# Optimization experiments

Measured on AMD Instinct MI355X. Metric: run time of the kernel, lower is better.

## Reference

```python
import jax, jax.numpy as jnp
import numpy as np

# ---- model hyperparameters (match init_kwargs) ----
N_ATOMS = 16000
N_EDGES = 256000
F = 128          # n_atom_basis
NF = 32          # n_filters
L = 3            # n_interactions
N_RBF = 20
CUTOFF = 5.0
MAX_Z = 100
INV_SQRT_F = np.float32(1.0 / np.sqrt(F))
INV_SQRT_2NF = np.float32(1.0 / np.sqrt(2 * NF))
SQ2 = np.float32(np.sqrt(2.0)); SQ3 = np.float32(np.sqrt(3.0)); SQ6 = np.float32(np.sqrt(6.0))
LOG2 = np.float32(np.log(2.0))


def ssp(x):
    # shifted softplus: softplus(x) - log(2)
    return jax.nn.softplus(x) - LOG2


def setup_inputs() -> dict:
    key = jax.random.key(0)
    k = jax.random.split(key, 16)
    Z = jax.random.randint(k[0], (N_ATOMS,), 0, MAX_Z)
    r_ij = jax.random.normal(k[1], (N_EDGES, 3), dtype=jnp.float32) * 2.0
    idx_i = jnp.sort(jax.random.randint(k[2], (N_EDGES,), 0, N_ATOMS))
    idx_j = jax.random.randint(k[3], (N_EDGES,), 0, N_ATOMS)
    # parameters (e3nn Linear: N(0,1) weights with explicit 1/sqrt(fan_in) in the math;
    # filter-network Dense: fan-in scaled weights, zero bias; padding_idx=0 -> zero row)
    emb = jax.random.normal(k[4], (MAX_Z, F), dtype=jnp.float32).at[0].set(0.0)
    W_pe = jax.random.normal(k[5], (F, F), dtype=jnp.float32)
    W0s = jax.random.normal(k[6], (L, F, NF), dtype=jnp.float32)   # in2f, 0e path
    W0v = jax.random.normal(k[7], (L, F, NF), dtype=jnp.float32)   # in2f, 1o path
    Wf1 = jax.random.normal(k[8], (L, N_RBF, NF), dtype=jnp.float32) / np.sqrt(N_RBF)
    bf1 = jnp.zeros((L, NF), jnp.float32)
    Wf2 = jax.random.normal(k[9], (L, NF, 6 * NF), dtype=jnp.float32) / np.sqrt(NF)
    bf2 = jnp.zeros((L, 6 * NF), jnp.float32)
    As = jax.random.normal(k[10], (L, 2 * NF, F), dtype=jnp.float32)  # f2out_1 0e
    Av = jax.random.normal(k[11], (L, 2 * NF, F), dtype=jnp.float32)  # f2out_1 1o
    Bs = jax.random.normal(k[12], (L, F, F), dtype=jnp.float32)       # f2out_2 0e
    Bv = jax.random.normal(k[13], (L, F, F), dtype=jnp.float32)       # f2out_2 1o
    return dict(Z=Z, r_ij=r_ij, idx_i=idx_i, idx_j=idx_j, emb=emb, W_pe=W_pe,
                W0s=W0s, W0v=W0v, Wf1=Wf1, bf1=bf1, Wf2=Wf2, bf2=bf2,
                As=As, Av=Av, Bs=Bs, Bv=Bv)


def _interaction(xs, xv, idx_i, idx_j, f_ij, rcut, Yv,
                 W0s, W0v, Wf1, bf1, Wf2, bf2, As, Av, Bs, Bv):
    n_atoms = xs.shape[0]
    # in2f: e3nn o3.Linear (per-l channel mixing, fan-in normalized)
    hs = (xs @ W0s) * INV_SQRT_F                        # [N, NF]  (0e)
    hv = jnp.einsum('nfc,fg->ngc', xv, W0v) * INV_SQRT_F  # [N, NF, 3] (1o)
    sj = hs[idx_j]                                      # gather neighbors [E, NF]
    vj = hv[idx_j]                                      # [E, NF, 3]
    # FullTensorProduct (0e+1o) x Y(0e+1o); Y0 = 1, Y1 = sqrt(3)*r_hat (component norm)
    Yb = Yv[:, None, :]                                 # [E, 1, 3]
    t0a = sj                                            # 0e x 0e -> 0e
    t0b = jnp.einsum('efc,ec->ef', vj, Yv) / SQ3        # 1o x 1o -> 0e
    t1a = sj[:, :, None] * Yb                           # 0e x 1o -> 1o
    t1b = vj                                            # 1o x 0e -> 1o
    t1e = jnp.cross(vj, Yb) / SQ2                       # 1o x 1o -> 1e
    ux, uy, uz = vj[..., 0], vj[..., 1], vj[..., 2]
    wx, wy, wz = Yv[:, None, 0], Yv[:, None, 1], Yv[:, None, 2]
    t2e = jnp.stack([(ux * wy + uy * wx) / SQ2,         # 1o x 1o -> 2e (sym traceless)
                     (uy * wz + uz * wy) / SQ2,
                     (2 * uz * wz - ux * wx - uy * wy) / SQ6,
                     (ux * wz + uz * wx) / SQ2,
                     (ux * wx - uy * wy) / SQ2], axis=-1)  # [E, NF, 5]
    # filter network + cutoff envelope: W_ij [E, 6*NF] (one scalar per irrep)
    W = (ssp(f_ij @ Wf1 + bf1) @ Wf2 + bf2) * rcut[:, None]
    w0a, w0b, w1a, w1b, w1e, w2e = jnp.split(W, 6, axis=1)
    E = sj.shape[0]
    # elementwise tensor product (scale each irrep by its scalar), then scatter-add
    y_all = jnp.concatenate([
        t0a * w0a, t0b * w0b,
        (t1a * w1a[..., None]).reshape(E, -1),
        (t1b * w1b[..., None]).reshape(E, -1),
        (t1e * w1e[..., None]).reshape(E, -1),
        (t2e * w2e[..., None]).reshape(E, -1)], axis=1)   # [E, 16*NF]
    agg = jax.ops.segment_sum(y_all, idx_i, num_segments=n_atoms)  # [N, 16*NF]
    s_in = agg[:, :2 * NF]
    v_in = agg[:, 2 * NF:8 * NF].reshape(n_atoms, 2 * NF, 3)
    # f2out_1: output irreps are F x (0e+1o) -> 1e and 2e channels have no path (dropped)
    os = ssp((s_in @ As) * INV_SQRT_2NF)                # f2out_1 + scalar activation
    ov = jnp.einsum('nfc,fg->ngc', v_in, Av) * INV_SQRT_2NF
    os = (os @ Bs) * INV_SQRT_F                         # f2out_2
    ov = jnp.einsum('nfc,fg->ngc', ov, Bv) * INV_SQRT_F
    return os, ov


def _forward(Z, r_ij, idx_i, idx_j, emb, W_pe, W0s, W0v, Wf1, bf1, Wf2, bf2, As, Av, Bs, Bv):
    xs = (emb[Z] @ W_pe) * INV_SQRT_F                   # embedding + post_embedding (0e)
    xv = jnp.zeros((xs.shape[0], F, 3), xs.dtype)       # 1o part starts at zero (no 0e->1o path)
    d = jnp.linalg.norm(r_ij, axis=1)
    offsets = jnp.linspace(0.0, CUTOFF, N_RBF).astype(jnp.float32)
    coeff = -0.5 / (offsets[1] - offsets[0]) ** 2
    f_ij = jnp.exp(coeff * (d[:, None] - offsets) ** 2)  # Gaussian RBF [E, N_RBF]
    rcut = 0.5 * (jnp.cos(np.float32(np.pi) * d / CUTOFF) + 1.0) * (d < CUTOFF)
    # spherical harmonics, normalize=True + component normalization (Y0=1, Y1=sqrt(3)*rhat);
    # the r_ij*rcut prescaling in the original doesn't change the direction, and edges with
    # rcut=0 contribute nothing since W_ij carries the rcut factor.
    Yv = SQ3 * r_ij / jnp.maximum(d, 1e-9)[:, None]
    for l in range(L):
        vs, vv = _interaction(xs, xv, idx_i, idx_j, f_ij, rcut, Yv,
                              W0s[l], W0v[l], Wf1[l], bf1[l], Wf2[l], bf2[l],
                              As[l], Av[l], Bs[l], Bv[l])
        xs = xs + vs
        xv = xv + vv
    return xs  # scalar_representation [N, F]


def reference(Z, r_ij, idx_i, idx_j, emb, W_pe, W0s, W0v, Wf1, bf1, Wf2, bf2, As, Av, Bs, Bv):
    return _forward(Z, r_ij, idx_i, idx_j, emb, W_pe, W0s, W0v, Wf1, bf1, Wf2, bf2, As, Av, Bs, Bv)
```

## Files before the change

### kernel.cpp

```cpp
#include <hip/hip_runtime.h>
#include <math.h>

constexpr int NA   = 16000;
constexpr int NE   = 256000;
constexpr int F    = 128;
constexpr int NF   = 32;
constexpr int NRBF = 20;
constexpr float CUTOFF       = 5.0f;
constexpr float INV_SQRT_F   = 0.0883883476483184f;
constexpr float INV_SQRT_2NF = 0.125f;
constexpr float INV_SQ3      = 0.5773502691896258f;
constexpr float SQ3          = 1.7320508075688772f;
constexpr float LOG2_        = 0.6931471805599453f;
constexpr float PI_          = 3.14159265358979323f;

typedef _Float16 h2 __attribute__((ext_vector_type(2)));

__device__ __forceinline__ float ssp(float x) {
    return fmaxf(x, 0.0f) + __logf(1.0f + __expf(-fabsf(x))) - LOG2_;
}
__device__ __forceinline__ float fdot2(h2 a, h2 b, float c) {
#if __has_builtin(__builtin_amdgcn_fdot2)
    return __builtin_amdgcn_fdot2(a, b, c, false);
#else
    return c + (float)a[0]*(float)b[0] + (float)a[1]*(float)b[1];
#endif
}

__global__ void geom_kernel(const float* __restrict__ r_ij,
                            float* __restrict__ fijT,
                            float* __restrict__ yvrT) {
    int e = blockIdx.x * blockDim.x + threadIdx.x;
    if (e >= NE) return;
    float x = r_ij[3*e+0], y = r_ij[3*e+1], z = r_ij[3*e+2];
    float d = sqrtf(x*x + y*y + z*z);
    const float delta = CUTOFF / (NRBF - 1);
    const float coeff = -0.5f / (delta * delta);
    #pragma unroll
    for (int k = 0; k < NRBF; k++) {
        float t = d - delta * (float)k;
        fijT[(size_t)k*NE + e] = __expf(coeff * t * t);
    }
    float rc = 0.5f * (__cosf(PI_ * d / CUTOFF) + 1.0f);
    rc = (d < CUTOFF) ? rc : 0.0f;
    float inv = SQ3 / fmaxf(d, 1e-9f);
    yvrT[0*(size_t)NE + e] = x * inv;
    yvrT[1*(size_t)NE + e] = y * inv;
    yvrT[2*(size_t)NE + e] = z * inv;
    yvrT[3*(size_t)NE + e] = rc;
}

__global__ void preph_kernel(const float* __restrict__ Wf2, const float* __restrict__ Wf1,
                             h2* __restrict__ Wf2H, h2* __restrict__ Wf1H) {
    int u = blockIdx.x * 256 + threadIdx.x;
    if (u < 3*128*16) {
        int l = u / (128*16), rem = u % (128*16), c = rem >> 4, k2 = rem & 15;
        const float* W = Wf2 + (size_t)l*NF*192;
        Wf2H[u] = h2{(_Float16)W[(2*k2)*192 + c], (_Float16)W[(2*k2+1)*192 + c]};
    }
    if (u < 3*320) {
        int l = u / 320, rem = u % 320, k2 = rem >> 5, g = rem & 31;
        const float* W = Wf1 + (size_t)l*NRBF*NF;
        Wf1H[u] = h2{(_Float16)W[(2*k2)*32 + g], (_Float16)W[(2*k2+1)*32 + g]};
    }
}

__global__ void prep2_kernel(const float* __restrict__ Av, const float* __restrict__ Bv,
                             float* __restrict__ AvBv) {
    int u = blockIdx.x * 256 + threadIdx.x;
    if (u >= 3*64*128) return;
    int l = u >> 13, rem = u & 8191, f = rem >> 7, c = rem & 127;
    const float* av = Av + (size_t)l*64*128 + f*128;
    const float* bv = Bv + (size_t)l*128*128 + c;
    float acc = 0.f;
    #pragma unroll 8
    for (int g = 0; g < 128; g++) acc += av[g] * bv[(size_t)g*128];
    AvBv[u] = acc * (INV_SQRT_2NF * INV_SQRT_F);
}

__global__ __launch_bounds__(256, 4)
void embed_kernel(const int* __restrict__ Z,
                  const float* __restrict__ emb,
                  const float* __restrict__ Wpe,
                  float* __restrict__ xs) {
    __shared__ float ER[32][128];
    __shared__ int   Zs[32];
    int t = threadIdx.x;
    int a0 = blockIdx.x * 32;
    if (t < 32) Zs[t] = Z[a0 + t];
    __syncthreads();
    {
        const float4* emb4 = (const float4*)emb;
        float4* ER4 = (float4*)&ER[0][0];
        #pragma unroll
        for (int it = 0; it < 4; it++) {
            int u4 = it*256 + t;
            int a = u4 >> 5, k4 = u4 & 31;
            ER4[u4] = emb4[(size_t)Zs[a]*32 + k4];
        }
    }
    __syncthreads();
    int c = t & 127, half = t >> 7;
    float acc[16];
    #pragma unroll
    for (int a = 0; a < 16; a++) acc[a] = 0.f;
    for (int k = 0; k < 128; k++) {
        float w = Wpe[k*128 + c];
        #pragma unroll
        for (int a = 0; a < 16; a++) acc[a] += ER[half*16 + a][k] * w;
    }
    #pragma unroll
    for (int a = 0; a < 16; a++)
        xs[(size_t)(a0 + half*16 + a)*128 + c] = acc[a] * INV_SQRT_F;
}

template <bool XV_ZERO>
__global__ __launch_bounds__(256, 4)
void h_kernel(const float* __restrict__ xs,
              const float* __restrict__ xv,
              const float* __restrict__ W0s,
              const float* __restrict__ W0v,
              float* __restrict__ hsv) {
    __shared__ float X[16][512];
    int t = threadIdx.x;
    int a0 = blockIdx.x * 16;
    {
        float* Xf = &X[0][0];
        const float4* xs4 = (const float4*)xs;
        #pragma unroll
        for (int it = 0; it < 2; it++) {
            int u4 = it*256 + t;
            int a = u4 >> 5, k4 = u4 & 31;
            *(float4*)&Xf[a*512 + k4*4] = xs4[(size_t)a0*32 + u4];
        }
        if (!XV_ZERO) {
            const float4* xv4 = (const float4*)xv;
            #pragma unroll
            for (int it = 0; it < 6; it++) {
                int u4 = it*256 + t;
                int a = u4 / 96, rem = u4 - a*96;
                *(float4*)&Xf[a*512 + 128 + rem*4] = xv4[(size_t)a0*96 + u4];
            }
        }
    }
    __syncthreads();
    int g = t & 31, r = t >> 5;
    int sel = r & 3, half = r >> 2;
    if (XV_ZERO && sel != 0) {
        #pragma unroll
        for (int a = 0; a < 8; a++) {
            int n = a0 + half*8 + a;
            hsv[(size_t)n*128 + 32 + g*3 + (sel-1)] = 0.f;
        }
        return;
    }
    const float* W = (sel == 0) ? W0s : W0v;
    int xoff = (sel == 0) ? 0 : (128 + (sel-1)*128);
    float acc[8];
    #pragma unroll
    for (int a = 0; a < 8; a++) acc[a] = 0.f;
    for (int k = 0; k < 128; k++) {
        float w = W[k*32 + g];
        #pragma unroll
        for (int a = 0; a < 8; a++) acc[a] += X[half*8 + a][xoff + k] * w;
    }
    #pragma unroll
    for (int a = 0; a < 8; a++) {
        int n = a0 + half*8 + a;
        if (sel == 0) hsv[(size_t)n*128 + g] = acc[a] * INV_SQRT_F;
        else          hsv[(size_t)n*128 + 32 + g*3 + (sel-1)] = acc[a] * INV_SQRT_F;
    }
}

template <bool DO_V>
__global__ __launch_bounds__(256, 6)
void agg_kernel(const int* __restrict__ idx_i,
                const int* __restrict__ idx_j,
                const float* __restrict__ fijT,
                const float* __restrict__ yvrT,
                const float* __restrict__ hsv,
                const h2* __restrict__ Wf1H,
                const float* __restrict__ bf1,
                const h2* __restrict__ Wf2H,
                const float* __restrict__ bf2,
                float* __restrict__ aggG) {
    __shared__ h2 LW1[320];
    __shared__ h2 HB[4][64][18];
    int t = threadIdx.x;
    for (int u = t; u < 320; u += 256) LW1[u] = Wf1H[u];
    __syncthreads();

    int wid = t >> 6, lane = t & 63;
    int base = (blockIdx.x*4 + wid) * 64;

    int   il = idx_i[base + lane];
    int   jl = idx_j[base + lane];
    float y0l = yvrT[0*(size_t)NE + base + lane];
    float y1l = yvrT[1*(size_t)NE + base + lane];
    float y2l = yvrT[2*(size_t)NE + base + lane];
    float y3l = yvrT[3*(size_t)NE + base + lane];

    int ilp = __shfl_up(il, 1);
    unsigned long long bmask = __ballot(lane > 0 && il != ilp);

    h2 fp[10];
    #pragma unroll
    for (int k2 = 0; k2 < 10; k2++) {
        float fa = fijT[(size_t)(2*k2)*NE + base + lane];
        float fb = fijT[(size_t)(2*k2+1)*NE + base + lane];
        fp[k2] = h2{(_Float16)fa, (_Float16)fb};
    }
    float h[32];
    #pragma unroll
    for (int g = 0; g < 32; g++) h[g] = bf1[g];
    #pragma unroll
    for (int k2 = 0; k2 < 10; k2++) {
        #pragma unroll
        for (int g = 0; g < 32; g++)
            h[g] = fdot2(fp[k2], LW1[k2*32 + g], h[g]);
    }
    #pragma unroll
    for (int g = 0; g < 32; g++) h[g] = ssp(h[g]);
    #pragma unroll
    for (int i = 0; i < 16; i++)
        HB[wid][lane][i] = h2{(_Float16)h[2*i], (_Float16)h[2*i+1]};

    h2 w2a[16], w2b[16];
    #pragma unroll
    for (int k2 = 0; k2 < 16; k2++) w2a[k2] = Wf2H[lane*16 + k2];
    if (DO_V) {
        #pragma unroll
        for (int k2 = 0; k2 < 16; k2++) w2b[k2] = Wf2H[(64+lane)*16 + k2];
    }
    float bf2a = bf2[lane];
    float bf2b = DO_V ? bf2[64 + lane] : 0.f;

    int idxQ = 32 + 3*(lane - 32);

    float a0 = 0.f, a1 = 0.f, a2 = 0.f, a3 = 0.f;
    int prev = __builtin_amdgcn_readlane(il, 0);

    for (int ii = 0; ii < 64; ++ii) {
        if ((bmask >> ii) & 1ull) {
            unsafeAtomicAdd(&aggG[(size_t)prev*256 + lane], a0);
            a0 = 0.f;
            if (DO_V) {
                unsafeAtomicAdd(&aggG[(size_t)prev*256 + 64 + lane],  a1);
                unsafeAtomicAdd(&aggG[(size_t)prev*256 + 128 + lane], a2);
                unsafeAtomicAdd(&aggG[(size_t)prev*256 + 192 + lane], a3);
                a1 = a2 = a3 = 0.f;
            }
            prev = __builtin_amdgcn_readlane(il, ii);
        }
        int j = __builtin_amdgcn_readlane(jl, ii);
        const float* row = hsv + (size_t)j*128;
        float q0, q1, q2;
        if (lane < 32) {
            q0 = row[lane]; q1 = q0; q2 = q0;
        } else {
            const float* p = row + idxQ;
            q0 = p[0]; q1 = p[1]; q2 = p[2];
        }
        float s0 = bf2a, s1 = bf2b;
        const h2* hrow = &HB[wid][ii][0];
        #pragma unroll
        for (int k2 = 0; k2 < 16; k2++) {
            h2 hq = hrow[k2];
            s0 = fdot2(hq, w2a[k2], s0);
            if (DO_V) s1 = fdot2(hq, w2b[k2], s1);
        }
        float y3s = __int_as_float(__builtin_amdgcn_readlane(__float_as_int(y3l), ii));
        float y0s = __int_as_float(__builtin_amdgcn_readlane(__float_as_int(y0l), ii));
        float y1s = __int_as_float(__builtin_amdgcn_readlane(__float_as_int(y1l), ii));
        float y2s = __int_as_float(__builtin_amdgcn_readlane(__float_as_int(y2l), ii));
        float w0 = s0 * y3s;
        float dot = (q0*y0s + q1*y1s + q2*y2s) * INV_SQ3;
        float v0 = (lane < 32) ? q0 : dot;
        a0 += v0 * w0;
        if (DO_V) {
            float w1 = s1 * y3s;
            float m1 = (lane < 32) ? y0s : 1.0f;
            float m2 = (lane < 32) ? y1s : 1.0f;
            float m3 = (lane < 32) ? y2s : 1.0f;
            a1 += q0 * m1 * w1;
            a2 += q1 * m2 * w1;
            a3 += q2 * m3 * w1;
        }
    }
    unsafeAtomicAdd(&aggG[(size_t)prev*256 + lane], a0);
    if (DO_V) {
        unsafeAtomicAdd(&aggG[(size_t)prev*256 + 64 + lane],  a1);
        unsafeAtomicAdd(&aggG[(size_t)prev*256 + 128 + lane], a2);
        unsafeAtomicAdd(&aggG[(size_t)prev*256 + 192 + lane], a3);
    }
}

template <bool DO_V, bool XV_WRITE>
__global__ __launch_bounds__(256, 4)
void mlp_kernel(const float* __restrict__ aggG,
                const float* __restrict__ As,
                const float* __restrict__ Bs,
                const float* __restrict__ AvBv,
                float* __restrict__ xs,
                float* __restrict__ xv) {
    constexpr int AC = DO_V ? 256 : 64;
    __shared__ float aggL[16][AC];
    __shared__ float outL[16][128];
    int t = threadIdx.x;
    int a0 = blockIdx.x * 16;
    {
        const float4* g4 = (const float4*)(aggG + (size_t)a0*256);
        if (DO_V) {
            float4* l4 = (float4*)&aggL[0][0];
            #pragma unroll
            for (int it = 0; it < 4; it++) l4[it*256 + t] = g4[it*256 + t];
        } else {
            int row = t >> 4, c4 = t & 15;
            *(float4*)&aggL[row][c4*4] = g4[row*64 + c4];
        }
    }
    __syncthreads();

    int q  = t & 31;
    int rp = t >> 5;
    const float4* As4 = (const float4*)As;
    const float4* Bs4 = (const float4*)Bs;

    {
        float ox0=0,oy0=0,oz0=0,ow0=0, ox1=0,oy1=0,oz1=0,ow1=0;
        const float4* x0p = (const float4*)&aggL[rp][0];
        const float4* x1p = (const float4*)&aggL[rp+8][0];
        #pragma unroll 4
        for (int kq = 0; kq < 16; kq++) {
            float4 x0 = x0p[kq], x1 = x1p[kq];
            float4 wa = As4[(4*kq+0)*32 + q];
            float4 wb = As4[(4*kq+1)*32 + q];
            float4 wc = As4[(4*kq+2)*32 + q];
            float4 wd = As4[(4*kq+3)*32 + q];
            ox0 += x0.x*wa.x + x0.y*wb.x + x0.z*wc.x + x0.w*wd.x;
            oy0 += x0.x*wa.y + x0.y*wb.y + x0.z*wc.y + x0.w*wd.y;
            oz0 += x0.x*wa.z + x0.y*wb.z + x0.z*wc.z + x0.w*wd.z;
            ow0 += x0.x*wa.w + x0.y*wb.w + x0.z*wc.w + x0.w*wd.w;
            ox1 += x1.x*wa.x + x1.y*wb.x + x1.z*wc.x + x1.w*wd.x;
            oy1 += x1.x*wa.y + x1.y*wb.y + x1.z*wc.y + x1.w*wd.y;
            oz1 += x1.x*wa.z + x1.y*wb.z + x1.z*wc.z + x1.w*wd.z;
            ow1 += x1.x*wa.w + x1.y*wb.w + x1.z*wc.w + x1.w*wd.w;
        }
        float4 r0 = { ssp(ox0*INV_SQRT_2NF), ssp(oy0*INV_SQRT_2NF), ssp(oz0*INV_SQRT_2NF), ssp(ow0*INV_SQRT_2NF) };
        float4 r1 = { ssp(ox1*INV_SQRT_2NF), ssp(oy1*INV_SQRT_2NF), ssp(oz1*INV_SQRT_2NF), ssp(ow1*INV_SQRT_2NF) };
        *(float4*)&outL[rp][4*q]   = r0;
        *(float4*)&outL[rp+8][4*q] = r1;
    }
    if (DO_V) {
        const float4* AB4 = (const float4*)AvBv;
        int ra[6], rc[6];
        #pragma unroll
        for (int i = 0; i < 6; i++) {
            int rv = rp + 8*i;
            ra[i] = rv/3; rc[i] = rv - 3*(rv/3);
        }
        float o[6][4];
        #pragma unroll
        for (int i = 0; i < 6; i++) { o[i][0]=0; o[i][1]=0; o[i][2]=0; o[i][3]=0; }
        const float4* vp[6];
        #pragma unroll
        for (int i = 0; i < 6; i++)
            vp[i] = (const float4*)&aggL[ra[i]][64 + rc[i]*64];
        #pragma unroll 2
        for (int kq = 0; kq < 16; kq++) {
            float4 wa = AB4[(4*kq+0)*32 + q];
            float4 wb = AB4[(4*kq+1)*32 + q];
            float4 wc = AB4[(4*kq+2)*32 + q];
            float4 wd = AB4[(4*kq+3)*32 + q];
            #pragma unroll
            for (int i = 0; i < 6; i++) {
                float4 x = vp[i][kq];
                o[i][0] += x.x*wa.x + x.y*wb.x + x.z*wc.x + x.w*wd.x;
                o[i][1] += x.x*wa.y + x.y*wb.y + x.z*wc.y + x.w*wd.y;
                o[i][2] += x.x*wa.z + x.y*wb.z + x.z*wc.z + x.w*wd.z;
                o[i][3] += x.x*wa.w + x.y*wb.w + x.z*wc.w + x.w*wd.w;
            }
        }
        #pragma unroll
        for (int i = 0; i < 6; i++) {
            float4* p = (float4*)&xv[(size_t)(a0+ra[i])*384 + rc[i]*128 + 4*q];
            if (XV_WRITE) {
                float4 c = { o[i][0], o[i][1], o[i][2], o[i][3] };
                *p = c;
            } else {
                float4 c = *p;
                c.x += o[i][0]; c.y += o[i][1]; c.z += o[i][2]; c.w += o[i][3];
                *p = c;
            }
        }
    }
    __syncthreads();
    {
        float ox0=0,oy0=0,oz0=0,ow0=0, ox1=0,oy1=0,oz1=0,ow1=0;
        const float4* x0p = (const float4*)&outL[rp][0];
        const float4* x1p = (const float4*)&outL[rp+8][0];
        #pragma unroll 4
        for (int kq = 0; kq < 32; kq++) {
            float4 x0 = x0p[kq], x1 = x1p[kq];
            float4 wa = Bs4[(4*kq+0)*32 + q];
            float4 wb = Bs4[(4*kq+1)*32 + q];
            float4 wc = Bs4[(4*kq+2)*32 + q];
            float4 wd = Bs4[(4*kq+3)*32 + q];
            ox0 += x0.x*wa.x + x0.y*wb.x + x0.z*wc.x + x0.w*wd.x;
            oy0 += x0.x*wa.y + x0.y*wb.y + x0.z*wc.y + x0.w*wd.y;
            oz0 += x0.x*wa.z + x0.y*wb.z + x0.z*wc.z + x0.w*wd.z;
            ow0 += x0.x*wa.w + x0.y*wb.w + x0.z*wc.w + x0.w*wd.w;
            ox1 += x1.x*wa.x + x1.y*wb.x + x1.z*wc.x + x1.w*wd.x;
            oy1 += x1.x*wa.y + x1.y*wb.y + x1.z*wc.y + x1.w*wd.y;
            oz1 += x1.x*wa.z + x1.y*wb.z + x1.z*wc.z + x1.w*wd.z;
            ow1 += x1.x*wa.w + x1.y*wb.w + x1.z*wc.w + x1.w*wd.w;
        }
        float4* p0 = (float4*)&xs[(size_t)(a0+rp)*128 + 4*q];
        float4* p1 = (float4*)&xs[(size_t)(a0+rp+8)*128 + 4*q];
        float4 c0 = *p0, c1 = *p1;
        c0.x += ox0*INV_SQRT_F; c0.y += oy0*INV_SQRT_F; c0.z += oz0*INV_SQRT_F; c0.w += ow0*INV_SQRT_F;
        c1.x += ox1*INV_SQRT_F; c1.y += oy1*INV_SQRT_F; c1.z += oz1*INV_SQRT_F; c1.w += ow1*INV_SQRT_F;
        *p0 = c0; *p1 = c1;
    }
}

extern "C" void kernel_launch(void* const* d_in, const int* in_sizes, int n_in,
                              void* d_out, int out_size, void* d_ws, size_t ws_size,
                              hipStream_t stream) {
    (void)in_sizes; (void)n_in; (void)out_size; (void)ws_size;
    const int*   Z     = (const int*)  d_in[0];
    const float* r_ij  = (const float*)d_in[1];
    const int*   idx_i = (const int*)  d_in[2];
    const int*   idx_j = (const int*)  d_in[3];
    const float* emb   = (const float*)d_in[4];
    const float* Wpe   = (const float*)d_in[5];
    const float* W0s   = (const float*)d_in[6];
    const float* W0v   = (const float*)d_in[7];
    const float* Wf1   = (const float*)d_in[8];
    const float* bf1   = (const float*)d_in[9];
    const float* Wf2   = (const float*)d_in[10];
    const float* bf2   = (const float*)d_in[11];
    const float* As    = (const float*)d_in[12];
    const float* Av    = (const float*)d_in[13];
    const float* Bs    = (const float*)d_in[14];
    const float* Bv    = (const float*)d_in[15];

    float* xs = (float*)d_out;
    float* ws = (float*)d_ws;
    float* fijT = ws;
    float* yvrT = fijT + (size_t)NE*NRBF;
    float* xv   = yvrT + (size_t)NE*4;
    float* hsv  = xv   + (size_t)NA*F*3;
    float* aggG = hsv  + (size_t)NA*F;
    float* AvBv = aggG + (size_t)NA*256;
    h2*    Wf2H = (h2*)(AvBv + (size_t)3*64*128);
    h2*    Wf1H = Wf2H + (size_t)3*128*16;

    geom_kernel<<<(NE+255)/256, 256, 0, stream>>>(r_ij, fijT, yvrT);
    preph_kernel<<<24, 256, 0, stream>>>(Wf2, Wf1, Wf2H, Wf1H);
    prep2_kernel<<<(3*64*128+255)/256, 256, 0, stream>>>(Av, Bv, AvBv);
    embed_kernel<<<NA/32, 256, 0, stream>>>(Z, emb, Wpe, xs);

    for (int l = 0; l < 3; l++) {
        if (l == 0)
            h_kernel<true><<<NA/16, 256, 0, stream>>>(xs, xv,
                W0s + (size_t)l*F*NF, W0v + (size_t)l*F*NF, hsv);
        else
            h_kernel<false><<<NA/16, 256, 0, stream>>>(xs, xv,
                W0s + (size_t)l*F*NF, W0v + (size_t)l*F*NF, hsv);

        hipMemsetAsync(aggG, 0, (size_t)NA*256*sizeof(float), stream);

        if (l < 2)
            agg_kernel<true><<<NE/256, 256, 0, stream>>>(idx_i, idx_j, fijT, yvrT, hsv,
                Wf1H + (size_t)l*320, bf1 + (size_t)l*NF,
                Wf2H + (size_t)l*128*16, bf2 + (size_t)l*6*NF, aggG);
        else
            agg_kernel<false><<<NE/256, 256, 0, stream>>>(idx_i, idx_j, fijT, yvrT, hsv,
                Wf1H + (size_t)l*320, bf1 + (size_t)l*NF,
                Wf2H + (size_t)l*128*16, bf2 + (size_t)l*6*NF, aggG);

        if (l == 0)
            mlp_kernel<true, true><<<NA/16, 256, 0, stream>>>(aggG,
                As + (size_t)l*2*NF*F, Bs + (size_t)l*F*F, AvBv + (size_t)l*64*128, xs, xv);
        else if (l == 1)
            mlp_kernel<true, false><<<NA/16, 256, 0, stream>>>(aggG,
                As + (size_t)l*2*NF*F, Bs + (size_t)l*F*F, AvBv + (size_t)l*64*128, xs, xv);
        else
            mlp_kernel<false, false><<<NA/16, 256, 0, stream>>>(aggG,
                As + (size_t)l*2*NF*F, Bs + (size_t)l*F*F, AvBv + (size_t)l*64*128, xs, xv);
    }
}
```

Before: 400.0 us.

## Fuse next-layer filter projection into embed and MLP kernels, vectorize agg row loads

Removes the separate h_kernel by computing the in2f projection (hsv) at the tail of embed_kernel for layer 0 and at the tail of mlp_kernel for later layers, reusing the freshly updated xs/xv rows already held in shared memory. This avoids re-reading xs and xv from global memory and saves three kernel launches. The agg kernel's per-edge filter hidden rows are also stored and read as 16-byte vectors. Launch bounds are relaxed (agg to 4 and mlp to 3 waves per SIMD), which may lower occupancy, and the mlp kernel grows in shared memory use and work per block.

New measurement: 402.8 us. Within noise of the previous version (+0.7%).

```diff
diff --git a/kernel.cpp b/kernel.cpp
--- a/kernel.cpp
+++ b/kernel.cpp
@@ -82,7 +82,9 @@
 void embed_kernel(const int* __restrict__ Z,
                   const float* __restrict__ emb,
                   const float* __restrict__ Wpe,
-                  float* __restrict__ xs) {
+                  const float* __restrict__ W0s,
+                  float* __restrict__ xs,
+                  float* __restrict__ hsv) {
     __shared__ float ER[32][128];
     __shared__ int   Zs[32];
     int t = threadIdx.x;
@@ -109,71 +111,36 @@
         #pragma unroll
         for (int a = 0; a < 16; a++) acc[a] += ER[half*16 + a][k] * w;
     }
-    #pragma unroll
-    for (int a = 0; a < 16; a++)
-        xs[(size_t)(a0 + half*16 + a)*128 + c] = acc[a] * INV_SQRT_F;
-}
-
-template <bool XV_ZERO>
+    __syncthreads();
+    #pragma unroll
+    for (int a = 0; a < 16; a++) {
+        float v = acc[a] * INV_SQRT_F;
+        xs[(size_t)(a0 + half*16 + a)*128 + c] = v;
+        ER[half*16 + a][c] = v;
+    }
+    __syncthreads();
+    {
+        int g = t & 31, rr = t >> 5;
+        float a2[4] = {0.f, 0.f, 0.f, 0.f};
+        for (int k = 0; k < 128; k++) {
+            float w = W0s[k*32 + g];
+            #pragma unroll
+            for (int a = 0; a < 4; a++) a2[a] += ER[rr*4 + a][k] * w;
+        }
+        #pragma unroll
+        for (int a = 0; a < 4; a++)
+            hsv[(size_t)(a0 + rr*4 + a)*128 + g] = a2[a] * INV_SQRT_F;
+        for (int u = t; u < 32*96; u += 256) {
+            int a = u / 96, rem = u - a*96;
+            hsv[(size_t)(a0 + a)*128 + 32 + rem] = 0.f;
+        }
+    }
+}
+
+struct alignas(16) HRow { h2 v[20]; };
+
+template <bool DO_V>
 __global__ __launch_bounds__(256, 4)
-void h_kernel(const float* __restrict__ xs,
-              const float* __restrict__ xv,
-              const float* __restrict__ W0s,
-              const float* __restrict__ W0v,
-              float* __restrict__ hsv) {
-    __shared__ float X[16][512];
-    int t = threadIdx.x;
-    int a0 = blockIdx.x * 16;
-    {
-        float* Xf = &X[0][0];
-        const float4* xs4 = (const float4*)xs;
-        #pragma unroll
-        for (int it = 0; it < 2; it++) {
-            int u4 = it*256 + t;
-            int a = u4 >> 5, k4 = u4 & 31;
-            *(float4*)&Xf[a*512 + k4*4] = xs4[(size_t)a0*32 + u4];
-        }
-        if (!XV_ZERO) {
-            const float4* xv4 = (const float4*)xv;
-            #pragma unroll
-            for (int it = 0; it < 6; it++) {
-                int u4 = it*256 + t;
-                int a = u4 / 96, rem = u4 - a*96;
-                *(float4*)&Xf[a*512 + 128 + rem*4] = xv4[(size_t)a0*96 + u4];
-            }
-        }
-    }
-    __syncthreads();
-    int g = t & 31, r = t >> 5;
-    int sel = r & 3, half = r >> 2;
-    if (XV_ZERO && sel != 0) {
-        #pragma unroll
-        for (int a = 0; a < 8; a++) {
-            int n = a0 + half*8 + a;
-            hsv[(size_t)n*128 + 32 + g*3 + (sel-1)] = 0.f;
-        }
-        return;
-    }
-    const float* W = (sel == 0) ? W0s : W0v;
-    int xoff = (sel == 0) ? 0 : (128 + (sel-1)*128);
-    float acc[8];
-    #pragma unroll
-    for (int a = 0; a < 8; a++) acc[a] = 0.f;
-    for (int k = 0; k < 128; k++) {
-        float w = W[k*32 + g];
-        #pragma unroll
-        for (int a = 0; a < 8; a++) acc[a] += X[half*8 + a][xoff + k] * w;
-    }
-    #pragma unroll
-    for (int a = 0; a < 8; a++) {
-        int n = a0 + half*8 + a;
-        if (sel == 0) hsv[(size_t)n*128 + g] = acc[a] * INV_SQRT_F;
-        else          hsv[(size_t)n*128 + 32 + g*3 + (sel-1)] = acc[a] * INV_SQRT_F;
-    }
-}
-
-template <bool DO_V>
-__global__ __launch_bounds__(256, 6)
 void agg_kernel(const int* __restrict__ idx_i,
                 const int* __restrict__ idx_j,
                 const float* __restrict__ fijT,
@@ -185,7 +152,7 @@
                 const float* __restrict__ bf2,
                 float* __restrict__ aggG) {
     __shared__ h2 LW1[320];
-    __shared__ h2 HB[4][64][18];
+    __shared__ HRow HB[4][64];
     int t = threadIdx.x;
     for (int u = t; u < 320; u += 256) LW1[u] = Wf1H[u];
     __syncthreads();
@@ -221,9 +188,15 @@
     }
     #pragma unroll
     for (int g = 0; g < 32; g++) h[g] = ssp(h[g]);
-    #pragma unroll
-    for (int i = 0; i < 16; i++)
-        HB[wid][lane][i] = h2{(_Float16)h[2*i], (_Float16)h[2*i+1]};
+    {
+        h2 hp[16];
+        #pragma unroll
+        for (int i = 0; i < 16; i++) hp[i] = h2{(_Float16)h[2*i], (_Float16)h[2*i+1]};
+        float4* dst = (float4*)HB[wid][lane].v;
+        const float4* srcp = (const float4*)hp;
+        #pragma unroll
+        for (int w = 0; w < 4; w++) dst[w] = srcp[w];
+    }
 
     h2 w2a[16], w2b[16];
     #pragma unroll
@@ -262,12 +235,16 @@
             q0 = p[0]; q1 = p[1]; q2 = p[2];
         }
         float s0 = bf2a, s1 = bf2b;
-        const h2* hrow = &HB[wid][ii][0];
-        #pragma unroll
-        for (int k2 = 0; k2 < 16; k2++) {
-            h2 hq = hrow[k2];
-            s0 = fdot2(hq, w2a[k2], s0);
-            if (DO_V) s1 = fdot2(hq, w2b[k2], s1);
+        {
+            const float4* hq4 = (const float4*)HB[wid][ii].v;
+            float4 bb[4];
+            bb[0] = hq4[0]; bb[1] = hq4[1]; bb[2] = hq4[2]; bb[3] = hq4[3];
+            const h2* hh = (const h2*)bb;
+            #pragma unroll
+            for (int k2 = 0; k2 < 16; k2++) {
+                s0 = fdot2(hh[k2], w2a[k2], s0);
+                if (DO_V) s1 = fdot2(hh[k2], w2b[k2], s1);
+            }
         }
         float y3s = __int_as_float(__builtin_amdgcn_readlane(__float_as_int(y3l), ii));
         float y0s = __int_as_float(__builtin_amdgcn_readlane(__float_as_int(y0l), ii));
@@ -295,17 +272,23 @@
     }
 }
 
-template <bool DO_V, bool XV_WRITE>
-__global__ __launch_bounds__(256, 4)
+template <bool DO_V, bool XV_WRITE, bool MAKE_H>
+__global__ __launch_bounds__(256, 3)
 void mlp_kernel(const float* __restrict__ aggG,
                 const float* __restrict__ As,
                 const float* __restrict__ Bs,
                 const float* __restrict__ AvBv,
+                const float* __restrict__ W0sN,
+                const float* __restrict__ W0vN,
                 float* __restrict__ xs,
-                float* __restrict__ xv) {
-    constexpr int AC = DO_V ? 256 : 64;
+                float* __restrict__ xv,
+                float* __restrict__ hsv) {
+    constexpr int AC  = DO_V ? 256 : 64;
+    constexpr int XR  = MAKE_H ? 16 : 1;
+    constexpr int XC  = MAKE_H ? 384 : 1;
     __shared__ float aggL[16][AC];
     __shared__ float outL[16][128];
+    __shared__ float xvL[XR][XC];
     int t = threadIdx.x;
     int a0 = blockIdx.x * 16;
     {
@@ -384,14 +367,15 @@
         #pragma unroll
         for (int i = 0; i < 6; i++) {
             float4* p = (float4*)&xv[(size_t)(a0+ra[i])*384 + rc[i]*128 + 4*q];
+            float4 c;
             if (XV_WRITE) {
-                float4 c = { o[i][0], o[i][1], o[i][2], o[i][3] };
-                *p = c;
+                c = make_float4(o[i][0], o[i][1], o[i][2], o[i][3]);
             } else {
-                float4 c = *p;
+                c = *p;
                 c.x += o[i][0]; c.y += o[i][1]; c.z += o[i][2]; c.w += o[i][3];
-                *p = c;
             }
+            *p = c;
+            if (MAKE_H) *(float4*)&xvL[ra[i]][rc[i]*128 + 4*q] = c;
         }
     }
     __syncthreads();
@@ -421,6 +405,34 @@
         c0.x += ox0*INV_SQRT_F; c0.y += oy0*INV_SQRT_F; c0.z += oz0*INV_SQRT_F; c0.w += ow0*INV_SQRT_F;
         c1.x += ox1*INV_SQRT_F; c1.y += oy1*INV_SQRT_F; c1.z += oz1*INV_SQRT_F; c1.w += ow1*INV_SQRT_F;
         *p0 = c0; *p1 = c1;
+        if (MAKE_H) {
+            *(float4*)&aggL[rp][4*q]   = c0;
+            *(float4*)&aggL[rp+8][4*q] = c1;
+        }
+    }
+    if (MAKE_H) {
+        __syncthreads();
+        int g = t & 31, r = t >> 5;
+        int sel = r & 3, half = r >> 2;
+        const float* W = (sel == 0) ? W0sN : W0vN;
+        const float* src;
+        int stride;
+        if (sel == 0) { src = &aggL[half*8][0];              stride = AC; }
+        else          { src = &xvL[half*8][(sel-1)*128];     stride = XC; }
+        float acc[8];
+        #pragma unroll
+        for (int a = 0; a < 8; a++) acc[a] = 0.f;
+        for (int k = 0; k < 128; k++) {
+            float w = W[k*32 + g];
+            #pragma unroll
+            for (int a = 0; a < 8; a++) acc[a] += src[a*stride + k] * w;
+        }
+        #pragma unroll
+        for (int a = 0; a < 8; a++) {
+            int n = a0 + half*8 + a;
+            if (sel == 0) hsv[(size_t)n*128 + g] = acc[a] * INV_SQRT_F;
+            else          hsv[(size_t)n*128 + 32 + g*3 + (sel-1)] = acc[a] * INV_SQRT_F;
+        }
     }
 }
 
@@ -459,16 +471,9 @@
     geom_kernel<<<(NE+255)/256, 256, 0, stream>>>(r_ij, fijT, yvrT);
     preph_kernel<<<24, 256, 0, stream>>>(Wf2, Wf1, Wf2H, Wf1H);
     prep2_kernel<<<(3*64*128+255)/256, 256, 0, stream>>>(Av, Bv, AvBv);
-    embed_kernel<<<NA/32, 256, 0, stream>>>(Z, emb, Wpe, xs);
+    embed_kernel<<<NA/32, 256, 0, stream>>>(Z, emb, Wpe, W0s, xs, hsv);
 
     for (int l = 0; l < 3; l++) {
-        if (l == 0)
-            h_kernel<true><<<NA/16, 256, 0, stream>>>(xs, xv,
-                W0s + (size_t)l*F*NF, W0v + (size_t)l*F*NF, hsv);
-        else
-            h_kernel<false><<<NA/16, 256, 0, stream>>>(xs, xv,
-                W0s + (size_t)l*F*NF, W0v + (size_t)l*F*NF, hsv);
-
         hipMemsetAsync(aggG, 0, (size_t)NA*256*sizeof(float), stream);
 
         if (l < 2)
@@ -481,13 +486,16 @@
                 Wf2H + (size_t)l*128*16, bf2 + (size_t)l*6*NF, aggG);
 
         if (l == 0)
-            mlp_kernel<true, true><<<NA/16, 256, 0, stream>>>(aggG,
-                As + (size_t)l*2*NF*F, Bs + (size_t)l*F*F, AvBv + (size_t)l*64*128, xs, xv);
+            mlp_kernel<true, true, true><<<NA/16, 256, 0, stream>>>(aggG,
+                As + (size_t)l*2*NF*F, Bs + (size_t)l*F*F, AvBv + (size_t)l*64*128,
+                W0s + (size_t)(l+1)*F*NF, W0v + (size_t)(l+1)*F*NF, xs, xv, hsv);
         else if (l == 1)
-            mlp_kernel<true, false><<<NA/16, 256, 0, stream>>>(aggG,
-                As + (size_t)l*2*NF*F, Bs + (size_t)l*F*F, AvBv + (size_t)l*64*128, xs, xv);
+            mlp_kernel<true, false, true><<<NA/16, 256, 0, stream>>>(aggG,
+                As + (size_t)l*2*NF*F, Bs + (size_t)l*F*F, AvBv + (size_t)l*64*128,
+                W0s + (size_t)(l+1)*F*NF, W0v + (size_t)(l+1)*F*NF, xs, xv, hsv);
         else
-            mlp_kernel<false, false><<<NA/16, 256, 0, stream>>>(aggG,
-                As + (size_t)l*2*NF*F, Bs + (size_t)l*F*F, AvBv + (size_t)l*64*128, xs, xv);
-    }
-}
+            mlp_kernel<false, false, false><<<NA/16, 256, 0, stream>>>(aggG,
+                As + (size_t)l*2*NF*F, Bs + (size_t)l*F*F, AvBv + (size_t)l*64*128,
+                W0s, W0v, xs, xv, hsv);
+    }
+}
```
